# Optimization experiments

Measured on AMD Instinct MI355X. Metric: run time of the kernel, lower is better.

Reference implementation:

```python
import jax, jax.numpy as jnp
import numpy as np
import math

B, S, H, D = 4, 4096, 2048, 128  # batch, seq_len, hidden_dim, head_size

def setup_inputs() -> dict:
    key = jax.random.key(0)
    ks = jax.random.split(key, 7)
    scale = 1.0 / math.sqrt(H)
    return {
        "x": jax.random.normal(ks[0], (B, S, H), dtype=jnp.float32),
        "Wq": jax.random.normal(ks[1], (H, D), dtype=jnp.float32) * scale,
        "bq": jnp.zeros((D,), dtype=jnp.float32),
        "Wk": jax.random.normal(ks[2], (H, D), dtype=jnp.float32) * scale,
        "bk": jnp.zeros((D,), dtype=jnp.float32),
        "Wv": jax.random.normal(ks[3], (H, D), dtype=jnp.float32) * scale,
        "bv": jnp.zeros((D,), dtype=jnp.float32),
    }

def reference(x, Wq, bq, Wk, bk, Wv, bv):
    # projections: [B,S,D]
    q = x @ Wq + bq
    k = x @ Wk + bk
    v = x @ Wv + bv
    # raw scores [B,S,S] with causal mask, NO pre-softmax scaling (as in source)
    scores = jnp.einsum('bsd,btd->bst', q, k)
    causal = jnp.tril(jnp.ones((S, S), dtype=bool))
    scores = jnp.where(causal, scores, -jnp.inf)
    # non-standard: scale AFTER softmax by 1/sqrt(head_size)
    w = jax.nn.softmax(scores, axis=-1) * (1.0 / math.sqrt(D))
    # dropout p=0.0 -> identity
    return jnp.einsum('bst,btd->bsd', w, v)
```

## Files before the change

### kernel.cpp

```cpp
#include <hip/hip_runtime.h>
#include <math.h>
#include <stdint.h>

#define SEQ   4096
#define HID   2048
#define HD    128
#define NROWS 16384

typedef __attribute__((ext_vector_type(8))) short bf16x8;
typedef __attribute__((ext_vector_type(4))) float f32x4;

static constexpr float OSCALE = 0.088388347648318447f;

using gvptr = const __attribute__((address_space(1))) void*;
using lvptr = __attribute__((address_space(3))) void*;
__device__ __forceinline__ void gld_lds16(const void* g, void* l) {
    __builtin_amdgcn_global_load_lds((gvptr)g, (lvptr)l, 16, 0, 0);
}

__device__ __forceinline__ unsigned short f2bf_rne(float f) {
    union { float f; unsigned u; } v; v.f = f;
    unsigned u = v.u + 0x7fffu + ((v.u >> 16) & 1u);
    return (unsigned short)(u >> 16);
}
__device__ __forceinline__ unsigned short f2bf_tr(float f) {
    union { float f; unsigned u; } v; v.f = f;
    return (unsigned short)(v.u >> 16);
}
__device__ __forceinline__ float bf2f(unsigned short h) {
    union { unsigned u; float f; } v; v.u = ((unsigned)h) << 16;
    return v.f;
}

__global__ __launch_bounds__(256) void prep_w(
    const float* __restrict__ Wq, const float* __restrict__ Wk, const float* __restrict__ Wv,
    unsigned short* __restrict__ wth, unsigned short* __restrict__ wtl)
{
    __shared__ float T[64][68];
    const int tid = threadIdx.x;
    const int k0 = blockIdx.x * 64, n0 = blockIdx.y * 64, mm = blockIdx.z;
    const float* W = (mm == 0) ? Wq : (mm == 1) ? Wk : Wv;
    #pragma unroll
    for (int i = 0; i < 4; ++i) {
        const int fi = i * 256 + tid, kk = fi >> 4, nc = (fi & 15) * 4;
        const float4 w = *(const float4*)(W + (size_t)(k0 + kk) * HD + n0 + nc);
        T[kk][nc] = w.x; T[kk][nc + 1] = w.y; T[kk][nc + 2] = w.z; T[kk][nc + 3] = w.w;
    }
    __syncthreads();
    unsigned short* oh = wth + (size_t)mm * HD * HID;
    unsigned short* ol = wtl + (size_t)mm * HD * HID;
    #pragma unroll
    for (int i = 0; i < 4; ++i) {
        const int fi = i * 256 + tid, nn = fi >> 4, kc = (fi & 15) * 4;
        const float a = T[kc][nn], b = T[kc + 1][nn], c = T[kc + 2][nn], d = T[kc + 3][nn];
        ushort4 hv, lv;
        hv.x = f2bf_rne(a); hv.y = f2bf_rne(b); hv.z = f2bf_rne(c); hv.w = f2bf_rne(d);
        lv.x = f2bf_rne(a - bf2f(hv.x)); lv.y = f2bf_rne(b - bf2f(hv.y));
        lv.z = f2bf_rne(c - bf2f(hv.z)); lv.w = f2bf_rne(d - bf2f(hv.w));
        *(ushort4*)(oh + (size_t)(n0 + nn) * HID + k0 + kc) = hv;
        *(ushort4*)(ol + (size_t)(n0 + nn) * HID + k0 + kc) = lv;
    }
}

__global__ __launch_bounds__(256, 3) void qkv_split(
    const float* __restrict__ x,
    const float* __restrict__ bq, const float* __restrict__ bk, const float* __restrict__ bv,
    const unsigned short* __restrict__ wth, const unsigned short* __restrict__ wtl,
    unsigned short* __restrict__ qh, unsigned short* __restrict__ ql,
    unsigned short* __restrict__ kh, unsigned short* __restrict__ kl,
    unsigned short* __restrict__ vth)
{
    __shared__ unsigned short Ah[64][64], Al[64][64];
    __shared__ unsigned short Bh[128][64], Bl[128][64];

    const int tid = threadIdx.x, wave = tid >> 6, lane = tid & 63;
    const int l15 = lane & 15, q4 = lane >> 4;
    const int wr = wave >> 1, wc = wave & 1;
    const int type = blockIdx.x % 3;
    const int tile = blockIdx.x / 3;
    const int r0 = tile * 64;
    const bool qk = (type < 2);

    const unsigned short* wh = wth + (size_t)type * HD * HID;
    const unsigned short* wl = wtl + (size_t)type * HD * HID;

    const int srow   = lane >> 3;
    const int schunk = ((lane & 7) ^ srow) * 8;

    f32x4 acc[2][4];
    #pragma unroll
    for (int mt = 0; mt < 2; ++mt)
        #pragma unroll
        for (int nt = 0; nt < 4; ++nt)
            acc[mt][nt] = (f32x4){0.f, 0.f, 0.f, 0.f};

    const float* xbase = x + (size_t)r0 * HID;

    float4 xv[4];
    #pragma unroll
    for (int i = 0; i < 4; ++i) {
        const int fi = i * 256 + tid, row = fi >> 4, kc = (fi & 15) * 4;
        xv[i] = *(const float4*)(xbase + (size_t)row * HID + kc);
    }

    for (int k0 = 0; k0 < HID; k0 += 64) {
        __syncthreads();

        {
            #pragma unroll
            for (int c = 0; c < 4; ++c) {
                const int row = wave * 32 + c * 8;
                gld_lds16(wh + (size_t)(row + srow) * HID + k0 + schunk, &Bh[row][0]);
            }
            if (qk) {
                #pragma unroll
                for (int c = 0; c < 4; ++c) {
                    const int row = wave * 32 + c * 8;
                    gld_lds16(wl + (size_t)(row + srow) * HID + k0 + schunk, &Bl[row][0]);
                }
            }
        }
        #pragma unroll
        for (int i = 0; i < 4; ++i) {
            const int fi = i * 256 + tid, row = fi >> 4, kc = (fi & 15) * 4;
            const int pk = ((kc >> 3) ^ (row & 7)) * 8 + (kc & 7);
            ushort4 hv;
            hv.x = f2bf_tr(xv[i].x); hv.y = f2bf_tr(xv[i].y);
            hv.z = f2bf_tr(xv[i].z); hv.w = f2bf_tr(xv[i].w);
            *(ushort4*)&Ah[row][pk] = hv;
            if (qk) {
                ushort4 lv;
                lv.x = f2bf_tr(xv[i].x - bf2f(hv.x)); lv.y = f2bf_tr(xv[i].y - bf2f(hv.y));
                lv.z = f2bf_tr(xv[i].z - bf2f(hv.z)); lv.w = f2bf_tr(xv[i].w - bf2f(hv.w));
                *(ushort4*)&Al[row][pk] = lv;
            }
        }
        __syncthreads();

        const int kn = (k0 + 64 < HID) ? (k0 + 64) : 0;
        #pragma unroll
        for (int i = 0; i < 4; ++i) {
            const int fi = i * 256 + tid, row = fi >> 4, kc = (fi & 15) * 4;
            xv[i] = *(const float4*)(xbase + (size_t)row * HID + kn + kc);
        }

        #pragma unroll
        for (int ks = 0; ks < 2; ++ks) {
            const int pc = ((ks * 4 + q4) ^ (l15 & 7)) * 8;
            bf16x8 ah[2], al[2];
            #pragma unroll
            for (int mt = 0; mt < 2; ++mt) {
                const int ar = wr * 32 + mt * 16 + l15;
                ah[mt] = *(const bf16x8*)&Ah[ar][pc];
                if (qk) al[mt] = *(const bf16x8*)&Al[ar][pc];
            }
            #pragma unroll
            for (int nt = 0; nt < 4; ++nt) {
                const int br = wc * 64 + nt * 16 + l15;
                const bf16x8 bh = *(const bf16x8*)&Bh[br][pc];
                #pragma unroll
                for (int mt = 0; mt < 2; ++mt)
                    acc[mt][nt] = __builtin_amdgcn_mfma_f32_16x16x32_bf16(ah[mt], bh, acc[mt][nt], 0, 0, 0);
                if (qk) {
                    const bf16x8 bl = *(const bf16x8*)&Bl[br][pc];
                    #pragma unroll
                    for (int mt = 0; mt < 2; ++mt) {
                        acc[mt][nt] = __builtin_amdgcn_mfma_f32_16x16x32_bf16(ah[mt], bl, acc[mt][nt], 0, 0, 0);
                        acc[mt][nt] = __builtin_amdgcn_mfma_f32_16x16x32_bf16(al[mt], bh, acc[mt][nt], 0, 0, 0);
                    }
                }
            }
        }
    }

    if (qk) {
        const float* bb = (type == 0) ? bq : bk;
        unsigned short* oh = (type == 0) ? qh : kh;
        unsigned short* ol = (type == 0) ? ql : kl;
        #pragma unroll
        for (int nt = 0; nt < 4; ++nt) {
            const int col = wc * 64 + nt * 16 + l15;
            const float bias = bb[col];
            #pragma unroll
            for (int mt = 0; mt < 2; ++mt) {
                const int Rb = r0 + wr * 32 + mt * 16 + q4 * 4;
                #pragma unroll
                for (int r = 0; r < 4; ++r) {
                    const float v = acc[mt][nt][r] + bias;
                    const unsigned short h = f2bf_rne(v);
                    oh[(size_t)(Rb + r) * HD + col] = h;
                    ol[(size_t)(Rb + r) * HD + col] = f2bf_rne(v - bf2f(h));
                }
            }
        }
    } else {
        #pragma unroll
        for (int nt = 0; nt < 4; ++nt) {
            const int col = wc * 64 + nt * 16 + l15;
            const float bias = bv[col];
            #pragma unroll
            for (int mt = 0; mt < 2; ++mt) {
                const int Rb = r0 + wr * 32 + mt * 16 + q4 * 4;
                const int bi = Rb >> 12, s0 = Rb & 4095;
                ushort4 pv;
                pv.x = f2bf_rne(acc[mt][nt][0] + bias);
                pv.y = f2bf_rne(acc[mt][nt][1] + bias);
                pv.z = f2bf_rne(acc[mt][nt][2] + bias);
                pv.w = f2bf_rne(acc[mt][nt][3] + bias);
                *(ushort4*)(vth + ((size_t)(bi * HD + col)) * SEQ + s0) = pv;
            }
        }
    }
}

__global__ __launch_bounds__(256, 3) void flash_mfma(
    const unsigned short* __restrict__ qh, const unsigned short* __restrict__ ql,
    const unsigned short* __restrict__ kh, const unsigned short* __restrict__ kl,
    const unsigned short* __restrict__ vth,
    unsigned short* __restrict__ oPb, float* __restrict__ mP, float* __restrict__ lP)
{
    __shared__ unsigned short Kh[64][128], Kl[64][128];
    __shared__ unsigned short Vt[128][64];

    const int tid = threadIdx.x, wave = tid >> 6, lane = tid & 63;
    const int l15 = lane & 15, q4 = lane >> 4;
    const int b = blockIdx.x & 3, h = (blockIdx.x >> 2) & 3, tord = blockIdx.x >> 4;
    const int tt = 63 - tord;
    const int n = tt + 1;
    const int j0 = (n * h) >> 2, j1 = (n * (h + 1)) >> 2;

    const int krow_l = lane >> 4;
    const int vrow_l = lane >> 3;
    const int vsc = ((lane & 7) ^ (vrow_l & 7)) * 8;
    const int kkey7 = l15 & 7;
    const int vkey7 = l15 & 7;

    const int qrow = b * SEQ + tt * 64 + wave * 16 + l15;
    bf16x8 aqh[4], aql[4];
    #pragma unroll
    for (int ks = 0; ks < 4; ++ks) {
        aqh[ks] = *(const bf16x8*)(qh + (size_t)qrow * HD + ks * 32 + q4 * 8);
        aql[ks] = *(const bf16x8*)(ql + (size_t)qrow * HD + ks * 32 + q4 * 8);
    }
    f32x4 oa[8];
    #pragma unroll
    for (int d = 0; d < 8; ++d) oa[d] = (f32x4){0.f, 0.f, 0.f, 0.f};
    float m_r = -INFINITY;
    float l_r = 0.f;

    for (int j = j0; j < j1; ++j) {
        __syncthreads();
        {
            const size_t kb = (size_t)b * SEQ + j * 64;
            #pragma unroll
            for (int c = 0; c < 4; ++c) {
                const int rl = c * 4 + krow_l;
                const int sc = (l15 ^ (rl & 7)) * 8;
                const size_t gr = (kb + wave * 16 + rl) * HD + sc;
                gld_lds16(kh + gr, &Kh[wave * 16 + c * 4][0]);
                gld_lds16(kl + gr, &Kl[wave * 16 + c * 4][0]);
            }
            #pragma unroll
            for (int c = 0; c < 4; ++c)
                gld_lds16(vth + ((size_t)(b * HD + wave * 32 + c * 8 + vrow_l)) * SEQ
                              + j * 64 + vsc,
                          &Vt[wave * 32 + c * 8][0]);
        }
        __syncthreads();

        f32x4 s[4];
        #pragma unroll
        for (int nt = 0; nt < 4; ++nt) s[nt] = (f32x4){0.f, 0.f, 0.f, 0.f};
        __builtin_amdgcn_s_setprio(1);
        #pragma unroll
        for (int ks = 0; ks < 4; ++ks) {
            const int pc = ((ks * 4 + q4) ^ kkey7) * 8;
            #pragma unroll
            for (int nt = 0; nt < 4; ++nt) {
                const bf16x8 bh = *(const bf16x8*)&Kh[nt * 16 + l15][pc];
                const bf16x8 bl = *(const bf16x8*)&Kl[nt * 16 + l15][pc];
                s[nt] = __builtin_amdgcn_mfma_f32_16x16x32_bf16(bh, aqh[ks], s[nt], 0, 0, 0);
                s[nt] = __builtin_amdgcn_mfma_f32_16x16x32_bf16(bh, aql[ks], s[nt], 0, 0, 0);
                s[nt] = __builtin_amdgcn_mfma_f32_16x16x32_bf16(bl, aqh[ks], s[nt], 0, 0, 0);
            }
        }
        __builtin_amdgcn_s_setprio(0);

        if (j == tt) {
            const int qloc = wave * 16 + l15;
            #pragma unroll
            for (int nt = 0; nt < 4; ++nt)
                #pragma unroll
                for (int r = 0; r < 4; ++r) {
                    const int kvl = nt * 16 + q4 * 4 + r;
                    if (kvl > qloc) s[nt][r] = -INFINITY;
                }
        }

        float mt = fmaxf(fmaxf(s[0][0], s[0][1]), fmaxf(s[0][2], s[0][3]));
        #pragma unroll
        for (int nt = 1; nt < 4; ++nt)
            mt = fmaxf(mt, fmaxf(fmaxf(s[nt][0], s[nt][1]), fmaxf(s[nt][2], s[nt][3])));
        mt = fmaxf(mt, __shfl_xor(mt, 16));
        mt = fmaxf(mt, __shfl_xor(mt, 32));

        const bool allskip = __all(mt <= m_r + 8.f);
        const float mn = allskip ? m_r : fmaxf(m_r, mt);

        f32x4 pf[4];
        #pragma unroll
        for (int nt = 0; nt < 4; ++nt)
            #pragma unroll
            for (int r = 0; r < 4; ++r)
                pf[nt][r] = __expf(s[nt][r] - mn);

        float ps = ((pf[0][0] + pf[0][1]) + (pf[0][2] + pf[0][3]))
                 + ((pf[1][0] + pf[1][1]) + (pf[1][2] + pf[1][3]))
                 + ((pf[2][0] + pf[2][1]) + (pf[2][2] + pf[2][3]))
                 + ((pf[3][0] + pf[3][1]) + (pf[3][2] + pf[3][3]));
        ps += __shfl_xor(ps, 16);
        ps += __shfl_xor(ps, 32);

        if (allskip) {
            l_r += ps;
        } else {
            const float al = __expf(m_r - mn);
            m_r = mn;
            l_r = l_r * al + ps;
            #pragma unroll
            for (int r = 0; r < 4; ++r) {
                const float alr = __shfl(al, (q4 << 2) | r);
                #pragma unroll
                for (int d = 0; d < 8; ++d) oa[d][r] *= alr;
            }
        }

        unsigned cc[4][2];
        #pragma unroll
        for (int nt = 0; nt < 4; ++nt) {
            cc[nt][0] = (unsigned)f2bf_tr(pf[nt][0]) | ((unsigned)f2bf_tr(pf[nt][1]) << 16);
            cc[nt][1] = (unsigned)f2bf_tr(pf[nt][2]) | ((unsigned)f2bf_tr(pf[nt][3]) << 16);
        }
        unsigned t0[2], t1[2], t2[2], t3[2];
        #pragma unroll
        for (int d = 0; d < 2; ++d) {
            t0[d] = (unsigned)__shfl_xor((int)cc[0][d], 16);
            t1[d] = (unsigned)__shfl_xor((int)cc[1][d], 16);
            t2[d] = (unsigned)__shfl_xor((int)cc[2][d], 16);
            t3[d] = (unsigned)__shfl_xor((int)cc[3][d], 16);
        }
        const bool ev = (q4 & 1) == 0;
        unsigned X0[2], X1[2], X2[2], X3[2];
        #pragma unroll
        for (int d = 0; d < 2; ++d) {
            X0[d] = ev ? cc[0][d] : t1[d];
            X1[d] = ev ? t0[d] : cc[1][d];
            X2[d] = ev ? cc[2][d] : t3[d];
            X3[d] = ev ? t2[d] : cc[3][d];
        }
        const int srcl = ((((q4 & 1) << 1) | (q4 >> 1)) << 4) | l15;
        union { unsigned u[4]; bf16x8 v; } A0, A1;
        A0.u[0] = (unsigned)__shfl((int)X0[0], srcl);
        A0.u[1] = (unsigned)__shfl((int)X0[1], srcl);
        A0.u[2] = (unsigned)__shfl((int)X1[0], srcl);
        A0.u[3] = (unsigned)__shfl((int)X1[1], srcl);
        A1.u[0] = (unsigned)__shfl((int)X2[0], srcl);
        A1.u[1] = (unsigned)__shfl((int)X2[1], srcl);
        A1.u[2] = (unsigned)__shfl((int)X3[0], srcl);
        A1.u[3] = (unsigned)__shfl((int)X3[1], srcl);

        __builtin_amdgcn_s_setprio(1);
        #pragma unroll
        for (int d = 0; d < 8; ++d) {
            const bf16x8 bv0 = *(const bf16x8*)&Vt[d * 16 + l15][(q4 ^ vkey7) * 8];
            const bf16x8 bv1 = *(const bf16x8*)&Vt[d * 16 + l15][((4 + q4) ^ vkey7) * 8];
            oa[d] = __builtin_amdgcn_mfma_f32_16x16x32_bf16(A0.v, bv0, oa[d], 0, 0, 0);
            oa[d] = __builtin_amdgcn_mfma_f32_16x16x32_bf16(A1.v, bv1, oa[d], 0, 0, 0);
        }
        __builtin_amdgcn_s_setprio(0);
    }

    const int R0 = b * SEQ + tt * 64 + wave * 16 + q4 * 4;
    unsigned short* op = oPb + (size_t)h * NROWS * HD;
    #pragma unroll
    for (int d = 0; d < 8; ++d)
        #pragma unroll
        for (int r = 0; r < 4; ++r)
            op[(size_t)(R0 + r) * HD + d * 16 + l15] = f2bf_rne(oa[d][r]);
    if (q4 == 0) {
        const int qr = b * SEQ + tt * 64 + wave * 16 + l15;
        mP[h * NROWS + qr] = m_r;
        lP[h * NROWS + qr] = l_r;
    }
}

__global__ __launch_bounds__(256) void flash_merge(
    const unsigned short* __restrict__ oPb, const float* __restrict__ mP,
    const float* __restrict__ lP, float* __restrict__ out)
{
    const int idx = blockIdx.x * 256 + threadIdx.x;
    const int r = idx >> 5, c = (idx & 31) * 4;
    float m[4], l[4];
    #pragma unroll
    for (int i = 0; i < 4; ++i) { m[i] = mP[i * NROWS + r]; l[i] = lP[i * NROWS + r]; }
    float M = fmaxf(fmaxf(m[0], m[1]), fmaxf(m[2], m[3]));
    float a[4], lsum = 0.f;
    #pragma unroll
    for (int i = 0; i < 4; ++i) { a[i] = __expf(m[i] - M); lsum += l[i] * a[i]; }
    const float inv = OSCALE / lsum;
    float ox = 0.f, oy = 0.f, oz = 0.f, ow = 0.f;
    #pragma unroll
    for (int i = 0; i < 4; ++i) {
        const ushort4 ov = *(const ushort4*)(oPb + (size_t)i * NROWS * HD + (size_t)r * HD + c);
        ox += a[i] * bf2f(ov.x); oy += a[i] * bf2f(ov.y);
        oz += a[i] * bf2f(ov.z); ow += a[i] * bf2f(ov.w);
    }
    float4 o; o.x = ox * inv; o.y = oy * inv; o.z = oz * inv; o.w = ow * inv;
    *(float4*)(out + (size_t)r * HD + c) = o;
}

extern "C" void kernel_launch(void* const* d_in, const int* in_sizes, int n_in,
                              void* d_out, int out_size, void* d_ws, size_t ws_size,
                              hipStream_t stream)
{
    (void)in_sizes; (void)n_in; (void)out_size; (void)ws_size;
    const float* x  = (const float*)d_in[0];
    const float* Wq = (const float*)d_in[1];
    const float* bq = (const float*)d_in[2];
    const float* Wk = (const float*)d_in[3];
    const float* bk = (const float*)d_in[4];
    const float* Wv = (const float*)d_in[5];
    const float* bv = (const float*)d_in[6];
    float* out = (float*)d_out;

    char* w = (char*)d_ws;
    unsigned short* qh  = (unsigned short*)(w);
    unsigned short* ql  = (unsigned short*)(w + 4194304);
    unsigned short* kh  = (unsigned short*)(w + 8388608);
    unsigned short* kl  = (unsigned short*)(w + 12582912);
    unsigned short* vth = (unsigned short*)(w + 16777216);
    unsigned short* wth = (unsigned short*)(w + 20971520);
    unsigned short* wtl = (unsigned short*)(w + 22544384);
    unsigned short* oPb = (unsigned short*)(w + 24117248);
    float* mP = (float*)(w + 40894464);
    float* lP = (float*)(w + 41156608);

    prep_w<<<dim3(32, 2, 3), 256, 0, stream>>>(Wq, Wk, Wv, wth, wtl);
    qkv_split<<<768, 256, 0, stream>>>(x, bq, bk, bv, wth, wtl, qh, ql, kh, kl, vth);
    flash_mfma<<<1024, 256, 0, stream>>>(qh, ql, kh, kl, vth, oPb, mP, lP);
    flash_merge<<<2048, 256, 0, stream>>>(oPb, mP, lP, out);
}
```

Before: 303.5 us.

## Double-buffer converted x tiles in LDS for QKV projection kernel

The qkv_split kernel now keeps two LDS buffers for the bf16 hi/lo x tiles. A prologue converts the first tile, and each iteration writes the next tile into the other buffer while MFMAs read the current one. The x prefetch distance grows to two tiles, and the launch-bounds occupancy hint drops from 3 to 2 blocks per CU to make room for the extra LDS. The aim is to overlap the x conversion and stores with the weight loads and compute. The costs are lower occupancy and an extra barrier per iteration.

```diff
diff --git a/kernel.cpp b/kernel.cpp
--- a/kernel.cpp
+++ b/kernel.cpp
@@ -62,7 +62,7 @@
     }
 }
 
-__global__ __launch_bounds__(256, 3) void qkv_split(
+__global__ __launch_bounds__(256, 2) void qkv_split(
     const float* __restrict__ x,
     const float* __restrict__ bq, const float* __restrict__ bk, const float* __restrict__ bv,
     const unsigned short* __restrict__ wth, const unsigned short* __restrict__ wtl,
@@ -70,7 +70,7 @@
     unsigned short* __restrict__ kh, unsigned short* __restrict__ kl,
     unsigned short* __restrict__ vth)
 {
-    __shared__ unsigned short Ah[64][64], Al[64][64];
+    __shared__ unsigned short Ah[2][64][64], Al[2][64][64];
     __shared__ unsigned short Bh[128][64], Bl[128][64];
 
     const int tid = threadIdx.x, wave = tid >> 6, lane = tid & 63;
@@ -102,8 +102,31 @@
         const int fi = i * 256 + tid, row = fi >> 4, kc = (fi & 15) * 4;
         xv[i] = *(const float4*)(xbase + (size_t)row * HID + kc);
     }
-
-    for (int k0 = 0; k0 < HID; k0 += 64) {
+    #pragma unroll
+    for (int i = 0; i < 4; ++i) {
+        const int fi = i * 256 + tid, row = fi >> 4, kc = (fi & 15) * 4;
+        const int pk = ((kc >> 3) ^ (row & 7)) * 8 + (kc & 7);
+        ushort4 hv;
+        hv.x = f2bf_tr(xv[i].x); hv.y = f2bf_tr(xv[i].y);
+        hv.z = f2bf_tr(xv[i].z); hv.w = f2bf_tr(xv[i].w);
+        *(ushort4*)&Ah[0][row][pk] = hv;
+        if (qk) {
+            ushort4 lv;
+            lv.x = f2bf_tr(xv[i].x - bf2f(hv.x)); lv.y = f2bf_tr(xv[i].y - bf2f(hv.y));
+            lv.z = f2bf_tr(xv[i].z - bf2f(hv.z)); lv.w = f2bf_tr(xv[i].w - bf2f(hv.w));
+            *(ushort4*)&Al[0][row][pk] = lv;
+        }
+    }
+    #pragma unroll
+    for (int i = 0; i < 4; ++i) {
+        const int fi = i * 256 + tid, row = fi >> 4, kc = (fi & 15) * 4;
+        xv[i] = *(const float4*)(xbase + (size_t)row * HID + 64 + kc);
+    }
+
+    for (int it = 0; it < 32; ++it) {
+        const int k0 = it * 64;
+        const int p = it & 1;
+
         __syncthreads();
 
         {
@@ -120,6 +143,9 @@
                 }
             }
         }
+
+        __syncthreads();
+
         #pragma unroll
         for (int i = 0; i < 4; ++i) {
             const int fi = i * 256 + tid, row = fi >> 4, kc = (fi & 15) * 4;
@@ -127,21 +153,21 @@
             ushort4 hv;
             hv.x = f2bf_tr(xv[i].x); hv.y = f2bf_tr(xv[i].y);
             hv.z = f2bf_tr(xv[i].z); hv.w = f2bf_tr(xv[i].w);
-            *(ushort4*)&Ah[row][pk] = hv;
+            *(ushort4*)&Ah[p ^ 1][row][pk] = hv;
             if (qk) {
                 ushort4 lv;
                 lv.x = f2bf_tr(xv[i].x - bf2f(hv.x)); lv.y = f2bf_tr(xv[i].y - bf2f(hv.y));
                 lv.z = f2bf_tr(xv[i].z - bf2f(hv.z)); lv.w = f2bf_tr(xv[i].w - bf2f(hv.w));
-                *(ushort4*)&Al[row][pk] = lv;
-            }
-        }
-        __syncthreads();
-
-        const int kn = (k0 + 64 < HID) ? (k0 + 64) : 0;
-        #pragma unroll
-        for (int i = 0; i < 4; ++i) {
-            const int fi = i * 256 + tid, row = fi >> 4, kc = (fi & 15) * 4;
-            xv[i] = *(const float4*)(xbase + (size_t)row * HID + kn + kc);
+                *(ushort4*)&Al[p ^ 1][row][pk] = lv;
+            }
+        }
+        {
+            const int kn = (k0 + 128) & (HID - 1);
+            #pragma unroll
+            for (int i = 0; i < 4; ++i) {
+                const int fi = i * 256 + tid, row = fi >> 4, kc = (fi & 15) * 4;
+                xv[i] = *(const float4*)(xbase + (size_t)row * HID + kn + kc);
+            }
         }
 
         #pragma unroll
@@ -151,8 +177,8 @@
             #pragma unroll
             for (int mt = 0; mt < 2; ++mt) {
                 const int ar = wr * 32 + mt * 16 + l15;
-                ah[mt] = *(const bf16x8*)&Ah[ar][pc];
-                if (qk) al[mt] = *(const bf16x8*)&Al[ar][pc];
+                ah[mt] = *(const bf16x8*)&Ah[p][ar][pc];
+                if (qk) al[mt] = *(const bf16x8*)&Al[p][ar][pc];
             }
             #pragma unroll
             for (int nt = 0; nt < 4; ++nt) {
```

Result: slower. 333.6 us (+9.9%).

## Double-buffer K tiles in LDS and prefetch the next tile during compute

Applied to the files above, without the earlier changes.

K hi/lo tiles now go into two LDS buffers: the first tile is loaded before the loop, and each iteration prefetches the next tile while computing on the current one. V is loaded at the top of each iteration. The two full __syncthreads are replaced by `s_waitcnt vmcnt` counts plus raw barriers, so each phase waits only for the loads it needs. The larger LDS footprint forces the occupancy hint down from 3 to 2 blocks per CU. That trades latency hiding across blocks for overlap within a block.

```diff
diff --git a/kernel.cpp b/kernel.cpp
--- a/kernel.cpp
+++ b/kernel.cpp
@@ -213,13 +213,13 @@
     }
 }
 
-__global__ __launch_bounds__(256, 3) void flash_mfma(
+__global__ __launch_bounds__(256, 2) void flash_mfma(
     const unsigned short* __restrict__ qh, const unsigned short* __restrict__ ql,
     const unsigned short* __restrict__ kh, const unsigned short* __restrict__ kl,
     const unsigned short* __restrict__ vth,
     unsigned short* __restrict__ oPb, float* __restrict__ mP, float* __restrict__ lP)
 {
-    __shared__ unsigned short Kh[64][128], Kl[64][128];
+    __shared__ unsigned short Kh2[2][64][128], Kl2[2][64][128];
     __shared__ unsigned short Vt[128][64];
 
     const int tid = threadIdx.x, wave = tid >> 6, lane = tid & 63;
@@ -248,25 +248,40 @@
     float m_r = -INFINITY;
     float l_r = 0.f;
 
+    if (j0 < j1) {
+        const size_t kb0 = (size_t)b * SEQ + j0 * 64;
+        #pragma unroll
+        for (int c = 0; c < 4; ++c) {
+            const int rl = c * 4 + krow_l;
+            const int sc = (l15 ^ (rl & 7)) * 8;
+            const size_t gr = (kb0 + wave * 16 + rl) * HD + sc;
+            gld_lds16(kh + gr, &Kh2[0][wave * 16 + c * 4][0]);
+            gld_lds16(kl + gr, &Kl2[0][wave * 16 + c * 4][0]);
+        }
+    }
+
+    int cur = 0;
     for (int j = j0; j < j1; ++j) {
-        __syncthreads();
+        #pragma unroll
+        for (int c = 0; c < 4; ++c)
+            gld_lds16(vth + ((size_t)(b * HD + wave * 32 + c * 8 + vrow_l)) * SEQ
+                          + j * 64 + vsc,
+                      &Vt[wave * 32 + c * 8][0]);
         {
-            const size_t kb = (size_t)b * SEQ + j * 64;
+            const int jn = (j + 1 < j1) ? (j + 1) : j;
+            const size_t kbn = (size_t)b * SEQ + jn * 64;
             #pragma unroll
             for (int c = 0; c < 4; ++c) {
                 const int rl = c * 4 + krow_l;
                 const int sc = (l15 ^ (rl & 7)) * 8;
-                const size_t gr = (kb + wave * 16 + rl) * HD + sc;
-                gld_lds16(kh + gr, &Kh[wave * 16 + c * 4][0]);
-                gld_lds16(kl + gr, &Kl[wave * 16 + c * 4][0]);
-            }
-            #pragma unroll
-            for (int c = 0; c < 4; ++c)
-                gld_lds16(vth + ((size_t)(b * HD + wave * 32 + c * 8 + vrow_l)) * SEQ
-                              + j * 64 + vsc,
-                          &Vt[wave * 32 + c * 8][0]);
-        }
-        __syncthreads();
+                const size_t gr = (kbn + wave * 16 + rl) * HD + sc;
+                gld_lds16(kh + gr, &Kh2[cur ^ 1][wave * 16 + c * 4][0]);
+                gld_lds16(kl + gr, &Kl2[cur ^ 1][wave * 16 + c * 4][0]);
+            }
+        }
+        asm volatile("s_waitcnt vmcnt(12)" ::: "memory");
+        __builtin_amdgcn_sched_barrier(0);
+        __builtin_amdgcn_s_barrier();
 
         f32x4 s[4];
         #pragma unroll
@@ -277,8 +292,8 @@
             const int pc = ((ks * 4 + q4) ^ kkey7) * 8;
             #pragma unroll
             for (int nt = 0; nt < 4; ++nt) {
-                const bf16x8 bh = *(const bf16x8*)&Kh[nt * 16 + l15][pc];
-                const bf16x8 bl = *(const bf16x8*)&Kl[nt * 16 + l15][pc];
+                const bf16x8 bh = *(const bf16x8*)&Kh2[cur][nt * 16 + l15][pc];
+                const bf16x8 bl = *(const bf16x8*)&Kl2[cur][nt * 16 + l15][pc];
                 s[nt] = __builtin_amdgcn_mfma_f32_16x16x32_bf16(bh, aqh[ks], s[nt], 0, 0, 0);
                 s[nt] = __builtin_amdgcn_mfma_f32_16x16x32_bf16(bh, aql[ks], s[nt], 0, 0, 0);
                 s[nt] = __builtin_amdgcn_mfma_f32_16x16x32_bf16(bl, aqh[ks], s[nt], 0, 0, 0);
@@ -334,6 +349,10 @@
                 for (int d = 0; d < 8; ++d) oa[d][r] *= alr;
             }
         }
+
+        asm volatile("s_waitcnt vmcnt(8)" ::: "memory");
+        __builtin_amdgcn_sched_barrier(0);
+        __builtin_amdgcn_s_barrier();
 
         unsigned cc[4][2];
         #pragma unroll
@@ -378,6 +397,9 @@
             oa[d] = __builtin_amdgcn_mfma_f32_16x16x32_bf16(A1.v, bv1, oa[d], 0, 0, 0);
         }
         __builtin_amdgcn_s_setprio(0);
+
+        __builtin_amdgcn_s_barrier();
+        cur ^= 1;
     }
 
     const int R0 = b * SEQ + tt * 64 + wave * 16 + q4 * 4;
```

Result: no change. 303.7 us (+0.1%).
